# Optimization experiments

Hardware: AMD Instinct MI355X
Metric: run time of the kernel (lower is better)

## Reference

```python
import jax, jax.numpy as jnp
import numpy as np

D_MODEL = 512
KEY_DIM = 128
TEMP = 30.0          # RelationUnit temperature
EPS = 1e-5           # InstanceL2Norm eps
SCALE = float(np.sqrt(1.0 / (D_MODEL * 4 * 4)))  # norm_scale in layers


def _sine_pos(hw, d, dtype=jnp.float32):
    # pos_seq = ones(hw).cumsum() -> 1..hw; outer with inv_freq; cat(sin, cos)
    pos = jnp.arange(1, hw + 1, dtype=dtype)
    inv_freq = 1.0 / (10000.0 ** (jnp.arange(0, d, 2, dtype=dtype) / d))
    ang = pos[:, None] * inv_freq[None, :]          # [hw, d/2]
    return jnp.concatenate([jnp.sin(ang), jnp.cos(ang)], axis=-1)  # [hw, d]


def _attn(q, k, v, wk, bk):
    # Single-head RelationUnit: shared WK projection, L2-normalize, temp softmax, raw value.
    # q: [Lq,B,D], k,v: [Lk,B,D]
    pq = q @ wk.T + bk
    pq = pq / jnp.maximum(jnp.linalg.norm(pq, axis=-1, keepdims=True), 1e-12)
    pk = k @ wk.T + bk
    pk = pk / jnp.maximum(jnp.linalg.norm(pk, axis=-1, keepdims=True), 1e-12)
    logits = jnp.einsum('qbe,kbe->bqk', pq, pk) * TEMP   # [B,Lq,Lk]
    a = jax.nn.softmax(logits, axis=-1)
    return jnp.einsum('bqk,kbd->qbd', a, v)


def _inorm(x, ni, b, d, h, w):
    # InstanceL2Norm (size_average=True) over (d,h,w) per (ni,b) sample.
    y = x.reshape(ni, h, w, b, d)
    ss = jnp.sum(y * y, axis=(1, 2, 4), keepdims=True)
    y = y * (SCALE * jnp.sqrt((d * h * w) / (ss + EPS)))
    return y.reshape(ni * h * w, b, d)


def _flatten(x5):
    # (ni,b,d,h,w) -> (ni*h*w, b, d), matching torch view/permute/reshape order.
    ni, b, d, h, w = x5.shape
    return x5.reshape(ni, b, d, h * w).transpose(0, 3, 1, 2).reshape(ni * h * w, b, d)


def _encoder(src5, pos5, wk, bk):
    ni, b, d, h, w = src5.shape
    x = _flatten(src5) + _flatten(pos5) * 1e-3
    x = x + _attn(x, x, x, wk, bk)
    return _inorm(x, ni, b, d, h, w)


def _decoder_one(tgt5, pos5, memory, pos, wk_s, bk_s, wk_c, bk_c):
    # Single decoder layer on one image (ni == 1).
    ni, b, d, h, w = tgt5.shape
    x = _flatten(tgt5) + _flatten(pos5) * 1e-3
    x = x + _attn(x, x, x, wk_s, bk_s)
    x = _inorm(x, ni, b, d, h, w)
    mask = _attn(x, memory, pos, wk_c, bk_c)
    t2 = _inorm(x * mask, ni, b, d, h, w)
    t3 = _attn(x, memory, memory * pos, wk_c, bk_c)
    t4 = _inorm(x + t3, ni, b, d, h, w)
    x = _inorm(t2 + t4, ni, b, d, h, w)
    return x.reshape(ni, h, w, b, d).transpose(0, 3, 4, 1, 2).reshape(ni * b, d, h, w)


def _forward(train_feat, test_feat, train_label, wk_self, bk_self, wk_cross, bk_cross):
    ntr, b, d, h, w = train_feat.shape
    nte = test_feat.shape[0]
    # Sinusoidal position embedding, reshaped to (d,h,w), broadcast over imgs/batch.
    pe = _sine_pos(h * w, d, train_feat.dtype).reshape(h, w, d).transpose(2, 0, 1)
    train_pos = jnp.broadcast_to(pe, (ntr, b, d, h, w))
    test_pos = jnp.broadcast_to(pe, (nte, b, d, h, w))
    memory = _encoder(train_feat, train_pos, wk_self, bk_self)   # [ntr*h*w, b, d]
    # label -> pos value sequence [ntr*h*w, b, d] (repeated over channel dim)
    pos = train_label.reshape(ntr, b, 1, h * w).transpose(0, 3, 1, 2).reshape(ntr * h * w, b, 1)
    pos = jnp.broadcast_to(pos, (ntr * h * w, b, d))

    def dec(t4, p4):
        return _decoder_one(t4[None], p4[None], memory, pos,
                            wk_self, bk_self, wk_cross, bk_cross)

    enc_feat = jax.vmap(dec)(train_feat, train_pos).reshape(ntr * b, d, h, w)
    dec_feat = jax.vmap(dec)(test_feat, test_pos).reshape(nte * b, d, h, w)
    return enc_feat, dec_feat


def setup_inputs() -> dict:
    key = jax.random.key(0)
    k1, k2, k3, k4, k5 = jax.random.split(key, 5)
    NTR, NTE, B, D, H, W = 3, 3, 16, 512, 22, 22
    std = float(np.sqrt(2.0 / D))  # kaiming-like init for WK
    return {
        'train_feat': jax.random.normal(k1, (NTR, B, D, H, W), jnp.float32),
        'test_feat': jax.random.normal(k2, (NTE, B, D, H, W), jnp.float32),
        'train_label': jax.random.uniform(k3, (NTR, B, H, W), jnp.float32),
        'wk_self': jax.random.normal(k4, (KEY_DIM, D), jnp.float32) * std,
        'bk_self': jnp.zeros((KEY_DIM,), jnp.float32),
        'wk_cross': jax.random.normal(k5, (KEY_DIM, D), jnp.float32) * std,
        'bk_cross': jnp.zeros((KEY_DIM,), jnp.float32),
    }


def reference(train_feat, test_feat, train_label, wk_self, bk_self, wk_cross, bk_cross):
    return _forward(train_feat, test_feat, train_label,
                    wk_self, bk_self, wk_cross, bk_cross)
```

## Files before the change

kernel.cpp:

```cpp
#include <hip/hip_runtime.h>
#include <math.h>

#define BATCH   16
#define DMODEL  512
#define EKEY    128
#define HWSZ    484
#define LENC    1452
#define LKPAD   1536
#define IMG_ELEMS (HWSZ*BATCH*DMODEL)
#define ENC_OUT   11894784ull
#define SQRT_TEMP 5.4772255750516611f
#define INORM_SCALE 0.011048543456039806f
#define NEGBIG   -3.0e38f

typedef _Float16 f16;
typedef _Float16 f16x8 __attribute__((ext_vector_type(8)));
typedef _Float16 f16x4 __attribute__((ext_vector_type(4)));
typedef float    f32x4 __attribute__((ext_vector_type(4)));

__device__ __forceinline__ f32x4 mfma16(f16x8 a, f16x8 b, f32x4 c) {
  return __builtin_amdgcn_mfma_f32_16x16x32_f16(a, b, c, 0, 0, 0);
}
__device__ __forceinline__ float inorm_coef(float ss) {
  return INORM_SCALE * sqrtf(247808.0f / (ss + 1e-5f));
}

#define BARRIER() do { asm volatile("s_waitcnt lgkmcnt(0)" ::: "memory"); \
                       __builtin_amdgcn_s_barrier();                      \
                       asm volatile("" ::: "memory"); } while (0)

__device__ __forceinline__ size_t vfrag_addr(size_t z, int nkt, int d, int k) {
  return (((z * 32 + (d >> 4)) * (size_t)nkt + (k >> 5)) << 9)
         + (((k >> 3) & 3) << 7) + ((d & 15) << 3) + (k & 7);
}

__global__ void init_zero_kernel(float* __restrict__ ss) { ss[threadIdx.x] = 0.0f; }

__global__ void peT_kernel(float* __restrict__ peT) {
  const int c = blockIdx.x;
  const int cc = (c < 256) ? c : c - 256;
  const float invf = 1.0f / powf(10000.0f, (float)(2 * cc) * (1.0f / 512.0f));
  for (int p = threadIdx.x; p < HWSZ; p += blockDim.x) {
    const float ang = (float)(p + 1) * invf;
    peT[c * HWSZ + p] = (c < 256) ? sinf(ang) : cosf(ang);
  }
}

__global__ void build_labelT_kernel(const float* __restrict__ lab, float* __restrict__ labT) {
  const int g = blockIdx.x;
  if (g < 48) {
    const int im = g >> 4, b = g & 15;
    for (int p = threadIdx.x; p < HWSZ; p += blockDim.x)
      labT[(size_t)b * LKPAD + im * HWSZ + p] = lab[((size_t)im * BATCH + b) * HWSZ + p];
  } else {
    const int b = g - 48;
    for (int p = LENC + threadIdx.x; p < LKPAD; p += blockDim.x)
      labT[(size_t)b * LKPAD + p] = 0.0f;
  }
}

__global__ void cvt16_kernel(const float* __restrict__ s, f16* __restrict__ d) {
  const int i = (blockIdx.x * 256 + threadIdx.x) * 4;
  const int r = i >> 9, c = i & 511;
  const float4 v = *(const float4*)(s + i);
  f16x4 h; h[0] = (f16)v.x; h[1] = (f16)v.y; h[2] = (f16)v.z; h[3] = (f16)v.w;
  f16* dp = d + ((((size_t)(r >> 4) << 4) + (c >> 5)) << 9)
              + (((c >> 3) & 3) << 7) + ((r & 15) << 3) + (c & 7);
  *(f16x4*)dp = h;
}

__global__ void vpad_kernel(f16* __restrict__ vt) {
  const int d = blockIdx.x, b = blockIdx.y;
  const int k = LENC + threadIdx.x;
  if (k < LKPAD) vt[vfrag_addr(b, 48, d, k)] = (f16)0.f;
}

__global__ __launch_bounds__(256) void build_input_kernel(
    const float* __restrict__ trainf, const float* __restrict__ testf,
    const float* __restrict__ peT, int i0, float* __restrict__ xout,
    f16* __restrict__ vt, int zmul, int col_im_step, int nkt)
{
  __shared__ float tile[32][33];
  const int tx = threadIdx.x, ty = threadIdx.y;
  const int pt = blockIdx.x * 32, ct = blockIdx.y * 32;
  const int im = blockIdx.z >> 4, b = blockIdx.z & 15;
  const int g = i0 + im;
  const float* src = (g < 3 ? trainf + (size_t)g * IMG_ELEMS
                            : testf + (size_t)(g - 3) * IMG_ELEMS)
                     + (size_t)b * (512 * 484);
  const int zv = zmul ? (im * 16 + b) : b;
  const int col0 = im * col_im_step;
#pragma unroll
  for (int j = 0; j < 4; ++j) {
    const int c = ct + ty + 8 * j, p = pt + tx;
    const int k = col0 + p;
    float val = 0.0f;
    if (p < HWSZ) {
      val = src[(size_t)c * 484 + p] + 1e-3f * peT[(size_t)c * 484 + p];
      vt[vfrag_addr(zv, nkt, c, k)] = (f16)val;
    } else if (zmul) {
      vt[vfrag_addr(zv, nkt, c, k)] = (f16)0.f;
    }
    tile[ty + 8 * j][tx] = val;
  }
  __syncthreads();
#pragma unroll
  for (int j = 0; j < 4; ++j) {
    const int p = pt + ty + 8 * j, c = ct + tx;
    if (p < HWSZ)
      xout[(((size_t)im * HWSZ + p) * BATCH + b) * DMODEL + c] = tile[tx][ty + 8 * j];
  }
}

__global__ __launch_bounds__(256) void v16t_mem_kernel(
    const float* __restrict__ src, const float* __restrict__ ssE, f16* __restrict__ dst)
{
  __shared__ f16 tile[32][33];
  const int tx = threadIdx.x, ty = threadIdx.y;
  const int l0 = blockIdx.x * 32, d0 = blockIdx.y * 32;
  const int b = blockIdx.z;
#pragma unroll
  for (int j = 0; j < 4; ++j) {
    const int l = l0 + ty + 8 * j;
    float v = 0.0f;
    if (l < LENC) {
      const float cf = inorm_coef(ssE[(l / 484) * 16 + b]);
      v = cf * src[((size_t)l * BATCH + b) * DMODEL + d0 + tx];
    }
    tile[ty + 8 * j][tx] = (f16)v;
  }
  __syncthreads();
#pragma unroll
  for (int j = 0; j < 4; ++j) {
    const int d = d0 + ty + 8 * j, l = l0 + tx;
    if (l < LKPAD) dst[vfrag_addr(b, 48, d, l)] = tile[tx][ty + 8 * j];
  }
}

__global__ __launch_bounds__(256) void proj_mfma_kernel(
    const float* __restrict__ X, const f16* __restrict__ W16,
    const float* __restrict__ bias, const float* __restrict__ ssg,
    f16* __restrict__ P16, int L, int NLT)
{
  __shared__ f16 Xs[64][72];
  const int t = threadIdx.x;
  const int wave = t >> 6, lane = t & 63, quad = lane >> 4, ln = lane & 15;
  const int lane8 = lane * 8;
  const size_t row0 = (size_t)blockIdx.x * 64;

  f32x4 acc[8];
#pragma unroll
  for (int nt = 0; nt < 8; ++nt) acc[nt] = (f32x4){0.f, 0.f, 0.f, 0.f};

  const int sr = t >> 2, sko = (t & 3) * 16;
  const size_t rowg = row0 + sr;
  float cf = 1.0f;
  if (ssg) {
    const int bb = (int)(rowg & 15);
    const int gg = (int)((rowg >> 4) / 484);
    cf = inorm_coef(ssg[gg * 16 + bb]);
  }
  const float* xp = X + rowg * 512 + sko;

  for (int k0 = 0; k0 < 512; k0 += 64) {
    {
      const float4 a0 = *(const float4*)(xp + k0);
      const float4 a1 = *(const float4*)(xp + k0 + 4);
      const float4 a2 = *(const float4*)(xp + k0 + 8);
      const float4 a3 = *(const float4*)(xp + k0 + 12);
      f16x8 h0, h1;
      h0[0]=(f16)(cf*a0.x); h0[1]=(f16)(cf*a0.y); h0[2]=(f16)(cf*a0.z); h0[3]=(f16)(cf*a0.w);
      h0[4]=(f16)(cf*a1.x); h0[5]=(f16)(cf*a1.y); h0[6]=(f16)(cf*a1.z); h0[7]=(f16)(cf*a1.w);
      h1[0]=(f16)(cf*a2.x); h1[1]=(f16)(cf*a2.y); h1[2]=(f16)(cf*a2.z); h1[3]=(f16)(cf*a2.w);
      h1[4]=(f16)(cf*a3.x); h1[5]=(f16)(cf*a3.y); h1[6]=(f16)(cf*a3.z); h1[7]=(f16)(cf*a3.w);
      *(f16x8*)&Xs[sr][sko]     = h0;
      *(f16x8*)&Xs[sr][sko + 8] = h1;
    }
    __syncthreads();
#pragma unroll
    for (int ks = 0; ks < 2; ++ks) {
      const f16x8 a = *(const f16x8*)&Xs[wave * 16 + ln][ks * 32 + quad * 8];
      const int kt = (k0 >> 5) + ks;
#pragma unroll
      for (int nt = 0; nt < 8; ++nt) {
        const f16x8 bf = *(const f16x8*)(W16 + (((size_t)(nt * 16 + kt)) << 9) + lane8);
        acc[nt] = mfma16(a, bf, acc[nt]);
      }
    }
    __syncthreads();
  }

  float bj[8];
#pragma unroll
  for (int nt = 0; nt < 8; ++nt) bj[nt] = bias[nt * 16 + ln];

  float y[8][4]; float ssq[4] = {0.f, 0.f, 0.f, 0.f};
#pragma unroll
  for (int nt = 0; nt < 8; ++nt)
#pragma unroll
    for (int r = 0; r < 4; ++r) {
      const float v = acc[nt][r] + bj[nt];
      y[nt][r] = v; ssq[r] = fmaf(v, v, ssq[r]);
    }
#pragma unroll
  for (int r = 0; r < 4; ++r) {
    ssq[r] += __shfl_xor(ssq[r], 1); ssq[r] += __shfl_xor(ssq[r], 2);
    ssq[r] += __shfl_xor(ssq[r], 4); ssq[r] += __shfl_xor(ssq[r], 8);
  }
#pragma unroll
  for (int r = 0; r < 4; ++r) {
    const float inv = SQRT_TEMP / fmaxf(sqrtf(ssq[r]), 1e-12f);
    const size_t rg = row0 + (size_t)wave * 16 + quad * 4 + r;
    const int b = (int)(rg & 15);
    const size_t lg = rg >> 4;
    const int im = (int)(lg / (size_t)L);
    const int l  = (int)(lg - (size_t)im * L);
    f16* zb = P16 + (((size_t)(im * 16 + b) * NLT + (l >> 4)) << 11) + ((l & 15) << 3) + (ln & 7);
#pragma unroll
    for (int nt = 0; nt < 8; ++nt)
      zb[((size_t)(nt >> 1) << 9) + (((nt * 2 + (ln >> 3)) & 3) << 7)] = (f16)(y[nt][r] * inv);
  }
}

template<int CROSS>
__global__ __launch_bounds__(512) void attn8_kernel(
    const f16* __restrict__ pq, const f16* __restrict__ pk, const f16* __restrict__ Vt,
    const float* __restrict__ labT, float* __restrict__ X, float* __restrict__ Vout,
    const float* __restrict__ ssIn, float* __restrict__ ssO,
    float* __restrict__ ssV_, float* __restrict__ ssUV_,
    int Lq, int Lk, int nqb, int nltq, int nltk, int nktv, int pk_shared, int vt_shared)
{
  __shared__ float Ssm[64][132];
  __shared__ f16   Psm[64][136];
  __shared__ float msh[64], lsh[64], ash[64], mask_sh[64];

  const int t = threadIdx.x;
  const int wave = t >> 6, lane = t & 63, quad = lane >> 4, ln = lane & 15;
  const int lane8 = lane * 8;

  const int id = blockIdx.x;
  const int b  = (id & 7) + 8 * ((id >> 3) & 1);
  const int jj = id >> 4;
  const int qb = jj % nqb, im = jj / nqb;
  const int q0 = qb * 64;
  const int zq = im * 16 + b;
  const int zk = pk_shared ? b : zq;
  const int zv = vt_shared ? b : zq;

  const f16* pqz = pq + (((size_t)zq * nltq) << 11);
  const f16* pkz = pk + (((size_t)zk * nltk) << 11);
  const f16* Vw  = Vt + ((((size_t)zv * 32 + wave * 4) * (size_t)nktv) << 9) + lane8;
  const float* ksb = CROSS ? labT + (size_t)b * LKPAD : (const float*)0;

  f16x8 qf[4][4];
#pragma unroll
  for (int mt = 0; mt < 4; ++mt) {
    const f16* qp = pqz + (((size_t)((q0 >> 4) + mt)) << 11) + lane8;
#pragma unroll
    for (int es = 0; es < 4; ++es) qf[mt][es] = *(const f16x8*)(qp + es * 512);
  }
  f16x8 kf[4];
  {
    const f16* kp = pkz + (((size_t)wave) << 11) + lane8;
#pragma unroll
    for (int es = 0; es < 4; ++es) kf[es] = *(const f16x8*)(kp + es * 512);
  }

  f32x4 oacc[4][4];
#pragma unroll
  for (int mt = 0; mt < 4; ++mt)
#pragma unroll
    for (int nt = 0; nt < 4; ++nt) oacc[mt][nt] = (f32x4){0.f, 0.f, 0.f, 0.f};

  if (t < 64) { msh[t] = NEGBIG; lsh[t] = 0.f; ash[t] = 0.f; }
  float msum = 0.f;
  const int qs = t >> 3, cs = t & 7;
  __syncthreads();

  const int nch = (Lk + 127) >> 7;

  for (int ch = 0; ch < nch; ++ch) {
    const int k0 = ch << 7;
    const int ktb = k0 >> 5;
    f16x8 bvA[4], bvB[4];
#pragma unroll
    for (int nt = 0; nt < 4; ++nt) {
      const f16* vpn = Vw + (((size_t)(nt * nktv + ktb)) << 9);
      bvA[nt] = *(const f16x8*)(vpn);
      bvB[nt] = *(const f16x8*)(vpn + 512);
    }
    float4 lv[4];
    if (CROSS) {
      const float* lp = ksb + k0 + cs * 16;
#pragma unroll
      for (int i = 0; i < 4; ++i) lv[i] = *(const float4*)(lp + i * 4);
    }
    {
      f32x4 s[4];
#pragma unroll
      for (int mt = 0; mt < 4; ++mt) s[mt] = (f32x4){0.f,0.f,0.f,0.f};
      __builtin_amdgcn_s_setprio(1);
#pragma unroll
      for (int es = 0; es < 4; ++es)
#pragma unroll
        for (int mt = 0; mt < 4; ++mt)
          s[mt] = mfma16(qf[mt][es], kf[es], s[mt]);
      __builtin_amdgcn_s_setprio(0);
#pragma unroll
      for (int mt = 0; mt < 4; ++mt)
#pragma unroll
        for (int r = 0; r < 4; ++r)
          Ssm[mt * 16 + quad * 4 + r][wave * 16 + ln] = s[mt][r];
    }
    if (ch + 1 < nch) {
      const f16* kp = pkz + (((size_t)(((ch + 1) << 3) + wave)) << 11) + lane8;
#pragma unroll
      for (int es = 0; es < 4; ++es) kf[es] = *(const f16x8*)(kp + es * 512);
    }
    BARRIER();
    {
      f32x4 sa[4];
#pragma unroll
      for (int i = 0; i < 4; ++i) sa[i] = *(const f32x4*)&Ssm[qs][cs * 16 + i * 4];
      float sv[16];
#pragma unroll
      for (int i = 0; i < 4; ++i)
#pragma unroll
        for (int j = 0; j < 4; ++j)
          sv[i * 4 + j] = sa[i][j];
      if (k0 + 128 > Lk) {
        const int kb = k0 + cs * 16;
#pragma unroll
        for (int j = 0; j < 16; ++j)
          if (kb + j >= Lk) sv[j] = NEGBIG;
      }
      float m8[8];
#pragma unroll
      for (int j = 0; j < 8; ++j) m8[j] = fmaxf(sv[j], sv[j + 8]);
      float m4[4];
#pragma unroll
      for (int j = 0; j < 4; ++j) m4[j] = fmaxf(m8[j], m8[j + 4]);
      float mx = fmaxf(fmaxf(m4[0], m4[2]), fmaxf(m4[1], m4[3]));
      mx = fmaxf(mx, __shfl_xor(mx, 1));
      mx = fmaxf(mx, __shfl_xor(mx, 2));
      mx = fmaxf(mx, __shfl_xor(mx, 4));
      const float mold = msh[qs];
      const float mnew = fmaxf(mold, mx);
      const float alpha = __expf(mold - mnew);
      float ps = 0.f, pm = 0.f;
      f16x8 pv0, pv1;
#pragma unroll
      for (int j = 0; j < 16; ++j) {
        float p = __expf(sv[j] - mnew);
        ps += p;
        if (CROSS) p *= lv[j >> 2][j & 3];
        pm += p;
        if (j < 8) pv0[j] = (f16)p; else pv1[j - 8] = (f16)p;
      }
      *(f16x8*)&Psm[qs][cs * 16]     = pv0;
      *(f16x8*)&Psm[qs][cs * 16 + 8] = pv1;
      ps += __shfl_xor(ps, 1); ps += __shfl_xor(ps, 2); ps += __shfl_xor(ps, 4);
      msum = msum * alpha + pm;
      if (cs == 0) { msh[qs] = mnew; lsh[qs] = lsh[qs] * alpha + ps; ash[qs] = alpha; }
    }
    BARRIER();
    {
      f16x8 bvC[4];
#pragma unroll
      for (int nt = 0; nt < 4; ++nt)
        bvC[nt] = *(const f16x8*)(Vw + (((size_t)(nt * nktv + ktb + 2)) << 9));
#pragma unroll
      for (int mt = 0; mt < 4; ++mt) {
        f32x4 al;
#pragma unroll
        for (int r = 0; r < 4; ++r) al[r] = ash[mt * 16 + quad * 4 + r];
#pragma unroll
        for (int nt = 0; nt < 4; ++nt) oacc[mt][nt] *= al;
      }
      f16x8 pa[4];
#pragma unroll
      for (int mt = 0; mt < 4; ++mt) pa[mt] = *(const f16x8*)&Psm[mt * 16 + ln][quad * 8];
      __builtin_amdgcn_s_setprio(1);
#pragma unroll
      for (int nt = 0; nt < 4; ++nt)
#pragma unroll
        for (int mt = 0; mt < 4; ++mt)
          oacc[mt][nt] = mfma16(pa[mt], bvA[nt], oacc[mt][nt]);
      __builtin_amdgcn_s_setprio(0);
      f16x8 bvD[4];
#pragma unroll
      for (int nt = 0; nt < 4; ++nt)
        bvD[nt] = *(const f16x8*)(Vw + (((size_t)(nt * nktv + ktb + 3)) << 9));
#pragma unroll
      for (int mt = 0; mt < 4; ++mt) pa[mt] = *(const f16x8*)&Psm[mt * 16 + ln][32 + quad * 8];
      __builtin_amdgcn_s_setprio(1);
#pragma unroll
      for (int nt = 0; nt < 4; ++nt)
#pragma unroll
        for (int mt = 0; mt < 4; ++mt)
          oacc[mt][nt] = mfma16(pa[mt], bvB[nt], oacc[mt][nt]);
      __builtin_amdgcn_s_setprio(0);
#pragma unroll
      for (int mt = 0; mt < 4; ++mt) pa[mt] = *(const f16x8*)&Psm[mt * 16 + ln][64 + quad * 8];
      __builtin_amdgcn_s_setprio(1);
#pragma unroll
      for (int nt = 0; nt < 4; ++nt)
#pragma unroll
        for (int mt = 0; mt < 4; ++mt)
          oacc[mt][nt] = mfma16(pa[mt], bvC[nt], oacc[mt][nt]);
      __builtin_amdgcn_s_setprio(0);
#pragma unroll
      for (int mt = 0; mt < 4; ++mt) pa[mt] = *(const f16x8*)&Psm[mt * 16 + ln][96 + quad * 8];
      __builtin_amdgcn_s_setprio(1);
#pragma unroll
      for (int nt = 0; nt < 4; ++nt)
#pragma unroll
        for (int mt = 0; mt < 4; ++mt)
          oacc[mt][nt] = mfma16(pa[mt], bvD[nt], oacc[mt][nt]);
      __builtin_amdgcn_s_setprio(0);
    }
  }

  if (CROSS) {
    float ms = msum;
    ms += __shfl_xor(ms, 1); ms += __shfl_xor(ms, 2); ms += __shfl_xor(ms, 4);
    if (cs == 0) mask_sh[qs] = ms / lsh[qs];
    __syncthreads();
  }

  const int g0  = (im * Lq + q0) / 484;
  const int bhi = (g0 + 1) * 484 - im * Lq;
  const bool strad = (!CROSS) && (bhi < Lq) && (bhi < q0 + 64);

  float a0 = 0.f, a1 = 0.f, a2 = 0.f;
  const float cfA = CROSS ? inorm_coef(ssIn[im * 16 + b]) : 0.f;

#pragma unroll
  for (int mt = 0; mt < 4; ++mt) {
    f32x4 li;
#pragma unroll
    for (int r = 0; r < 4; ++r) li[r] = 1.0f / lsh[mt * 16 + quad * 4 + r];
#pragma unroll
    for (int r = 0; r < 4; ++r) {
      const int q = q0 + mt * 16 + quad * 4 + r;
      if (q < Lq) {
        const size_t base = (((size_t)(im * Lq + q)) * BATCH + b) * DMODEL + wave * 64 + ln;
        if (!CROSS) {
          const bool hi = (q >= bhi);
#pragma unroll
          for (int nt = 0; nt < 4; ++nt) {
            const float y = X[base + nt * 16] + oacc[mt][nt][r] * li[r];
            X[base + nt * 16] = y;
            if (hi) a1 += y * y; else a0 += y * y;
          }
        } else {
          const float mval = mask_sh[mt * 16 + quad * 4 + r];
#pragma unroll
          for (int nt = 0; nt < 4; ++nt) {
            const float x1 = cfA * X[base + nt * 16];
            const float u = x1 * mval;
            const float v = x1 + oacc[mt][nt][r] * li[r];
            X[base + nt * 16] = u;
            Vout[base + nt * 16] = v;
            a0 += u * u; a1 += v * v; a2 += u * v;
          }
        }
      }
    }
  }
#pragma unroll
  for (int m = 32; m; m >>= 1) {
    a0 += __shfl_xor(a0, m); a1 += __shfl_xor(a1, m);
    if (CROSS) a2 += __shfl_xor(a2, m);
  }
  if (lane == 0) {
    if (!CROSS) {
      atomicAdd(ssO + g0 * 16 + b, a0);
      if (strad) atomicAdd(ssO + (g0 + 1) * 16 + b, a1);
    } else {
      const int g = im * 16 + b;
      atomicAdd(ssO + g, a0);
      atomicAdd(ssV_ + g, a1);
      atomicAdd(ssUV_ + g, a2);
    }
  }
}

__global__ void coef_final_kernel(const float* __restrict__ ssU, const float* __restrict__ ssV,
                                  const float* __restrict__ ssUV, float* __restrict__ AB, int n)
{
  const int t = threadIdx.x;
  if (t < n) {
    const float su = ssU[t], sv = ssV[t], suv = ssUV[t];
    const float cu = inorm_coef(su), cv = inorm_coef(sv);
    const float ssz = cu * cu * su + cv * cv * sv + 2.f * cu * cv * suv;
    const float cz = inorm_coef(ssz);
    AB[2 * t] = cu * cz; AB[2 * t + 1] = cv * cz;
  }
}

__global__ __launch_bounds__(256) void final_out_kernel(
    const float* __restrict__ u, const float* __restrict__ v,
    const float* __restrict__ AB, float* __restrict__ out, int i0)
{
  __shared__ float tile[32][33];
  const int tx = threadIdx.x, ty = threadIdx.y;
  const int pt = blockIdx.x * 32, ct = blockIdx.y * 32;
  const int z = blockIdx.z;
  const int im = z >> 4, b = z & 15;
  const float A = AB[2 * z], B = AB[2 * z + 1];
#pragma unroll
  for (int j = 0; j < 4; ++j) {
    const int p = pt + ty + 8 * j, c = ct + tx;
    float val = 0.0f;
    if (p < HWSZ) {
      const size_t idx = (((size_t)im * HWSZ + p) * BATCH + b) * DMODEL + c;
      val = A * u[idx] + B * v[idx];
    }
    tile[ty + 8 * j][tx] = val;
  }
  __syncthreads();
  const int g = i0 + im;
  const size_t base = (g < 3 ? 0ull : ENC_OUT)
                    + ((size_t)(((g < 3 ? g : g - 3) * 16 + b) * 512)) * 484ull;
#pragma unroll
  for (int j = 0; j < 4; ++j) {
    const int c = ct + ty + 8 * j, p = pt + tx;
    if (p < HWSZ) out[base + (size_t)c * 484 + p] = tile[tx][ty + 8 * j];
  }
}

extern "C" void kernel_launch(void* const* d_in, const int* in_sizes, int n_in,
                              void* d_out, int out_size, void* d_ws, size_t ws_size,
                              hipStream_t stream) {
  (void)in_sizes; (void)n_in; (void)out_size;
  const float* train_feat  = (const float*)d_in[0];
  const float* test_feat   = (const float*)d_in[1];
  const float* train_label = (const float*)d_in[2];
  const float* wk_self     = (const float*)d_in[3];
  const float* bk_self     = (const float*)d_in[4];
  const float* wk_cross    = (const float*)d_in[5];
  const float* bk_cross    = (const float*)d_in[6];
  float* out = (float*)d_out;
  char* wsb  = (char*)d_ws;

  size_t off = 0;
  auto alloc = [&](size_t bytes) { size_t r = off; off = (r + bytes + 255) & ~(size_t)255; return r; };
  const size_t o_peT   = alloc(991232ull);
  const size_t o_labT  = alloc(16ull * LKPAD * 4);
  const size_t o_ss    = alloc(4096);
  const size_t o_w16s  = alloc(131072);
  const size_t o_w16c  = alloc(131072);
  const size_t o_xenc  = alloc(47579136ull);
  const size_t o_p16   = alloc(6291456ull);
  const size_t o_vte   = alloc(16ull*512*LKPAD*2);
  const size_t o_vtm   = alloc(16ull*512*LKPAD*2);
  const size_t fixed = off;

  float* peT  = (float*)(wsb + o_peT);
  float* labT = (float*)(wsb + o_labT);
  float* ss   = (float*)(wsb + o_ss);
  f16*   w16s = (f16*)(wsb + o_w16s);
  f16*   w16c = (f16*)(wsb + o_w16c);
  float* xenc = (float*)(wsb + o_xenc);
  f16*   p16  = (f16*)(wsb + o_p16);
  f16*   vte  = (f16*)(wsb + o_vte);
  f16*   vtm  = (f16*)(wsb + o_vtm);
  float* ssE = ss, *ssA = ss + 128, *ssU = ss + 256, *ssV = ss + 384, *ssUV = ss + 512;
  float* AB  = ss + 640;

  const size_t decPer = 15859712ull * 2 + 2097152ull + 8388608ull;
  int NB = 6;
  if (fixed + (size_t)NB * decPer + 4096 > ws_size) NB = 3;
  if (fixed + (size_t)NB * decPer + 4096 > ws_size) NB = 1;

  float* xd    = (float*)(wsb + fixed);
  float* vbuf  = xd + (size_t)NB * IMG_ELEMS;
  f16*   pq16d = (f16*)(vbuf + (size_t)NB * IMG_ELEMS);
  f16*   vtd   = pq16d + (size_t)NB * 1048576ull;

  init_zero_kernel<<<dim3(1), dim3(1024), 0, stream>>>(ss);
  peT_kernel<<<dim3(512), dim3(256), 0, stream>>>(peT);
  build_labelT_kernel<<<dim3(64), dim3(256), 0, stream>>>(train_label, labT);
  cvt16_kernel<<<dim3(64), dim3(256), 0, stream>>>(wk_self, w16s);
  cvt16_kernel<<<dim3(64), dim3(256), 0, stream>>>(wk_cross, w16c);
  vpad_kernel<<<dim3(512, 16), dim3(96), 0, stream>>>(vte);

  build_input_kernel<<<dim3(16, 16, 48), dim3(32, 8), 0, stream>>>(
      train_feat, test_feat, peT, 0, xenc, vte, 0, 484, 48);
  proj_mfma_kernel<<<dim3(363), dim3(256), 0, stream>>>(xenc, w16s, bk_self, (const float*)0, p16, LENC, 96);
  attn8_kernel<0><<<dim3(23 * 16), dim3(512), 0, stream>>>(
      p16, p16, vte, (const float*)0, xenc, (float*)0, (const float*)0,
      ssE, (float*)0, (float*)0, LENC, LENC, 23, 96, 96, 48, 0, 0);
  proj_mfma_kernel<<<dim3(363), dim3(256), 0, stream>>>(xenc, w16c, bk_cross, ssE, p16, LENC, 96);
  v16t_mem_kernel<<<dim3(48, 16, 16), dim3(32, 8), 0, stream>>>(xenc, ssE, vtm);

  for (int i0 = 0; i0 < 6; i0 += NB) {
    build_input_kernel<<<dim3(16, 16, NB * 16), dim3(32, 8), 0, stream>>>(
        train_feat, test_feat, peT, i0, xd, vtd, 1, 0, 16);
    proj_mfma_kernel<<<dim3(NB * 121), dim3(256), 0, stream>>>(xd, w16s, bk_self, (const float*)0, pq16d, HWSZ, 32);
    attn8_kernel<0><<<dim3(8 * 16 * NB), dim3(512), 0, stream>>>(
        pq16d, pq16d, vtd, (const float*)0, xd, (float*)0, (const float*)0,
        ssA + i0 * 16, (float*)0, (float*)0, HWSZ, HWSZ, 8, 32, 32, 16, 0, 0);
    proj_mfma_kernel<<<dim3(NB * 121), dim3(256), 0, stream>>>(xd, w16c, bk_cross, ssA + i0 * 16, pq16d, HWSZ, 32);
    attn8_kernel<1><<<dim3(8 * 16 * NB), dim3(512), 0, stream>>>(
        pq16d, p16 , vtm, labT, xd, vbuf, ssA + i0 * 16,
        ssU + i0 * 16, ssV + i0 * 16, ssUV + i0 * 16, HWSZ, LENC, 8, 32, 96, 48, 1, 1);
    coef_final_kernel<<<dim3(1), dim3(128), 0, stream>>>(
        ssU + i0 * 16, ssV + i0 * 16, ssUV + i0 * 16, AB + i0 * 32, NB * 16);
    final_out_kernel<<<dim3(16, 16, NB * 16), dim3(32, 8), 0, stream>>>(
        xd, vbuf, AB + i0 * 32, out, i0);
  }
}
```

Before: 899.3 us.

## Software-pipeline attention loop with double-buffered score and probability tiles

```diff
diff --git a/kernel.cpp b/kernel.cpp
--- a/kernel.cpp
+++ b/kernel.cpp
@@ -223,16 +223,16 @@
 }
 
 template<int CROSS>
-__global__ __launch_bounds__(512) void attn8_kernel(
+__global__ __launch_bounds__(512) void attn9_kernel(
     const f16* __restrict__ pq, const f16* __restrict__ pk, const f16* __restrict__ Vt,
     const float* __restrict__ labT, float* __restrict__ X, float* __restrict__ Vout,
     const float* __restrict__ ssIn, float* __restrict__ ssO,
     float* __restrict__ ssV_, float* __restrict__ ssUV_,
     int Lq, int Lk, int nqb, int nltq, int nltk, int nktv, int pk_shared, int vt_shared)
 {
-  __shared__ float Ssm[64][132];
-  __shared__ f16   Psm[64][136];
-  __shared__ float msh[64], lsh[64], ash[64], mask_sh[64];
+  __shared__ float Ssm[2][64][132];
+  __shared__ f16   Psm[2][64][136];
+  __shared__ float msh[64], lsh[64], ash[2][64], mask_sh[64];
 
   const int t = threadIdx.x;
   const int wave = t >> 6, lane = t & 63, quad = lane >> 4, ln = lane & 15;
@@ -272,30 +272,119 @@
 #pragma unroll
     for (int nt = 0; nt < 4; ++nt) oacc[mt][nt] = (f32x4){0.f, 0.f, 0.f, 0.f};
 
-  if (t < 64) { msh[t] = NEGBIG; lsh[t] = 0.f; ash[t] = 0.f; }
+  if (t < 64) { msh[t] = NEGBIG; lsh[t] = 0.f; }
   float msum = 0.f;
   const int qs = t >> 3, cs = t & 7;
-  __syncthreads();
 
   const int nch = (Lk + 127) >> 7;
 
-  for (int ch = 0; ch < nch; ++ch) {
-    const int k0 = ch << 7;
-    const int ktb = k0 >> 5;
-    f16x8 bvA[4], bvB[4];
-#pragma unroll
-    for (int nt = 0; nt < 4; ++nt) {
-      const f16* vpn = Vw + (((size_t)(nt * nktv + ktb)) << 9);
-      bvA[nt] = *(const f16x8*)(vpn);
-      bvB[nt] = *(const f16x8*)(vpn + 512);
-    }
+  {
+    f32x4 s[4];
+#pragma unroll
+    for (int mt = 0; mt < 4; ++mt) s[mt] = (f32x4){0.f,0.f,0.f,0.f};
+    __builtin_amdgcn_s_setprio(1);
+#pragma unroll
+    for (int es = 0; es < 4; ++es)
+#pragma unroll
+      for (int mt = 0; mt < 4; ++mt)
+        s[mt] = mfma16(qf[mt][es], kf[es], s[mt]);
+    __builtin_amdgcn_s_setprio(0);
+#pragma unroll
+    for (int mt = 0; mt < 4; ++mt)
+#pragma unroll
+      for (int r = 0; r < 4; ++r)
+        Ssm[0][mt * 16 + quad * 4 + r][wave * 16 + ln] = s[mt][r];
+  }
+  if (nch > 1) {
+    const f16* kp = pkz + (((size_t)(8 + wave)) << 11) + lane8;
+#pragma unroll
+    for (int es = 0; es < 4; ++es) kf[es] = *(const f16x8*)(kp + es * 512);
+  }
+  f16x8 bvA[4], bvB[4], bvC[4], bvD[4];
+  BARRIER();
+
+  for (int i = 0; i < nch; ++i) {
+    const int buf = i & 1;
+    const int k0 = i << 7;
+    const int ktb = i << 2;
+    f32x4 sa[4];
+#pragma unroll
+    for (int ii = 0; ii < 4; ++ii) sa[ii] = *(const f32x4*)&Ssm[buf][qs][cs * 16 + ii * 4];
     float4 lv[4];
     if (CROSS) {
       const float* lp = ksb + k0 + cs * 16;
 #pragma unroll
-      for (int i = 0; i < 4; ++i) lv[i] = *(const float4*)(lp + i * 4);
-    }
-    {
+      for (int ii = 0; ii < 4; ++ii) lv[ii] = *(const float4*)(lp + ii * 4);
+    }
+    if (i) {
+#pragma unroll
+      for (int mt = 0; mt < 4; ++mt) {
+        f32x4 al;
+#pragma unroll
+        for (int r = 0; r < 4; ++r) al[r] = ash[buf ^ 1][mt * 16 + quad * 4 + r];
+#pragma unroll
+        for (int nt = 0; nt < 4; ++nt) oacc[mt][nt] *= al;
+      }
+      f16x8 pa[4];
+#pragma unroll
+      for (int mt = 0; mt < 4; ++mt) pa[mt] = *(const f16x8*)&Psm[buf ^ 1][mt * 16 + ln][quad * 8];
+      __builtin_amdgcn_s_setprio(1);
+#pragma unroll
+      for (int nt = 0; nt < 4; ++nt)
+#pragma unroll
+        for (int mt = 0; mt < 4; ++mt)
+          oacc[mt][nt] = mfma16(pa[mt], bvA[nt], oacc[mt][nt]);
+      __builtin_amdgcn_s_setprio(0);
+#pragma unroll
+      for (int nt = 0; nt < 4; ++nt)
+        bvA[nt] = *(const f16x8*)(Vw + (((size_t)(nt * nktv + ktb)) << 9));
+#pragma unroll
+      for (int mt = 0; mt < 4; ++mt) pa[mt] = *(const f16x8*)&Psm[buf ^ 1][mt * 16 + ln][32 + quad * 8];
+      __builtin_amdgcn_s_setprio(1);
+#pragma unroll
+      for (int nt = 0; nt < 4; ++nt)
+#pragma unroll
+        for (int mt = 0; mt < 4; ++mt)
+          oacc[mt][nt] = mfma16(pa[mt], bvB[nt], oacc[mt][nt]);
+      __builtin_amdgcn_s_setprio(0);
+#pragma unroll
+      for (int nt = 0; nt < 4; ++nt)
+        bvB[nt] = *(const f16x8*)(Vw + (((size_t)(nt * nktv + ktb + 1)) << 9));
+#pragma unroll
+      for (int mt = 0; mt < 4; ++mt) pa[mt] = *(const f16x8*)&Psm[buf ^ 1][mt * 16 + ln][64 + quad * 8];
+      __builtin_amdgcn_s_setprio(1);
+#pragma unroll
+      for (int nt = 0; nt < 4; ++nt)
+#pragma unroll
+        for (int mt = 0; mt < 4; ++mt)
+          oacc[mt][nt] = mfma16(pa[mt], bvC[nt], oacc[mt][nt]);
+      __builtin_amdgcn_s_setprio(0);
+#pragma unroll
+      for (int nt = 0; nt < 4; ++nt)
+        bvC[nt] = *(const f16x8*)(Vw + (((size_t)(nt * nktv + ktb + 2)) << 9));
+#pragma unroll
+      for (int mt = 0; mt < 4; ++mt) pa[mt] = *(const f16x8*)&Psm[buf ^ 1][mt * 16 + ln][96 + quad * 8];
+      __builtin_amdgcn_s_setprio(1);
+#pragma unroll
+      for (int nt = 0; nt < 4; ++nt)
+#pragma unroll
+        for (int mt = 0; mt < 4; ++mt)
+          oacc[mt][nt] = mfma16(pa[mt], bvD[nt], oacc[mt][nt]);
+      __builtin_amdgcn_s_setprio(0);
+#pragma unroll
+      for (int nt = 0; nt < 4; ++nt)
+        bvD[nt] = *(const f16x8*)(Vw + (((size_t)(nt * nktv + ktb + 3)) << 9));
+    } else {
+#pragma unroll
+      for (int nt = 0; nt < 4; ++nt) {
+        const f16* vpn = Vw + (((size_t)(nt * nktv)) << 9);
+        bvA[nt] = *(const f16x8*)(vpn);
+        bvB[nt] = *(const f16x8*)(vpn + 512);
+        bvC[nt] = *(const f16x8*)(vpn + 1024);
+        bvD[nt] = *(const f16x8*)(vpn + 1536);
+      }
+    }
+    if (i + 1 < nch) {
       f32x4 s[4];
 #pragma unroll
       for (int mt = 0; mt < 4; ++mt) s[mt] = (f32x4){0.f,0.f,0.f,0.f};
@@ -310,24 +399,20 @@
       for (int mt = 0; mt < 4; ++mt)
 #pragma unroll
         for (int r = 0; r < 4; ++r)
-          Ssm[mt * 16 + quad * 4 + r][wave * 16 + ln] = s[mt][r];
-    }
-    if (ch + 1 < nch) {
-      const f16* kp = pkz + (((size_t)(((ch + 1) << 3) + wave)) << 11) + lane8;
-#pragma unroll
-      for (int es = 0; es < 4; ++es) kf[es] = *(const f16x8*)(kp + es * 512);
-    }
-    BARRIER();
+          Ssm[buf ^ 1][mt * 16 + quad * 4 + r][wave * 16 + ln] = s[mt][r];
+      if (i + 2 < nch) {
+        const f16* kp = pkz + (((size_t)(((i + 2) << 3) + wave)) << 11) + lane8;
+#pragma unroll
+        for (int es = 0; es < 4; ++es) kf[es] = *(const f16x8*)(kp + es * 512);
+      }
+    }
     {
-      f32x4 sa[4];
-#pragma unroll
-      for (int i = 0; i < 4; ++i) sa[i] = *(const f32x4*)&Ssm[qs][cs * 16 + i * 4];
       float sv[16];
 #pragma unroll
-      for (int i = 0; i < 4; ++i)
+      for (int ii = 0; ii < 4; ++ii)
 #pragma unroll
         for (int j = 0; j < 4; ++j)
-          sv[i * 4 + j] = sa[i][j];
+          sv[ii * 4 + j] = sa[ii][j];
       if (k0 + 128 > Lk) {
         const int kb = k0 + cs * 16;
 #pragma unroll
@@ -357,66 +442,38 @@
         pm += p;
         if (j < 8) pv0[j] = (f16)p; else pv1[j - 8] = (f16)p;
       }
-      *(f16x8*)&Psm[qs][cs * 16]     = pv0;
-      *(f16x8*)&Psm[qs][cs * 16 + 8] = pv1;
+      *(f16x8*)&Psm[buf][qs][cs * 16]     = pv0;
+      *(f16x8*)&Psm[buf][qs][cs * 16 + 8] = pv1;
       ps += __shfl_xor(ps, 1); ps += __shfl_xor(ps, 2); ps += __shfl_xor(ps, 4);
       msum = msum * alpha + pm;
-      if (cs == 0) { msh[qs] = mnew; lsh[qs] = lsh[qs] * alpha + ps; ash[qs] = alpha; }
+      if (cs == 0) { msh[qs] = mnew; lsh[qs] = lsh[qs] * alpha + ps; ash[buf][qs] = alpha; }
     }
     BARRIER();
-    {
-      f16x8 bvC[4];
-#pragma unroll
-      for (int nt = 0; nt < 4; ++nt)
-        bvC[nt] = *(const f16x8*)(Vw + (((size_t)(nt * nktv + ktb + 2)) << 9));
-#pragma unroll
-      for (int mt = 0; mt < 4; ++mt) {
-        f32x4 al;
-#pragma unroll
-        for (int r = 0; r < 4; ++r) al[r] = ash[mt * 16 + quad * 4 + r];
-#pragma unroll
-        for (int nt = 0; nt < 4; ++nt) oacc[mt][nt] *= al;
-      }
-      f16x8 pa[4];
-#pragma unroll
-      for (int mt = 0; mt < 4; ++mt) pa[mt] = *(const f16x8*)&Psm[mt * 16 + ln][quad * 8];
+  }
+
+  {
+    const int bl = (nch - 1) & 1;
+#pragma unroll
+    for (int mt = 0; mt < 4; ++mt) {
+      f32x4 al;
+#pragma unroll
+      for (int r = 0; r < 4; ++r) al[r] = ash[bl][mt * 16 + quad * 4 + r];
+#pragma unroll
+      for (int nt = 0; nt < 4; ++nt) oacc[mt][nt] *= al;
+    }
+    f16x8 pa[4];
+#pragma unroll
+    for (int ks = 0; ks < 4; ++ks) {
+#pragma unroll
+      for (int mt = 0; mt < 4; ++mt) pa[mt] = *(const f16x8*)&Psm[bl][mt * 16 + ln][ks * 32 + quad * 8];
       __builtin_amdgcn_s_setprio(1);
 #pragma unroll
-      for (int nt = 0; nt < 4; ++nt)
+      for (int nt = 0; nt < 4; ++nt) {
+        const f16x8 bv = (ks == 0) ? bvA[nt] : (ks == 1) ? bvB[nt] : (ks == 2) ? bvC[nt] : bvD[nt];
 #pragma unroll
         for (int mt = 0; mt < 4; ++mt)
-          oacc[mt][nt] = mfma16(pa[mt], bvA[nt], oacc[mt][nt]);
-      __builtin_amdgcn_s_setprio(0);
-      f16x8 bvD[4];
-#pragma unroll
-      for (int nt = 0; nt < 4; ++nt)
-        bvD[nt] = *(const f16x8*)(Vw + (((size_t)(nt * nktv + ktb + 3)) << 9));
-#pragma unroll
-      for (int mt = 0; mt < 4; ++mt) pa[mt] = *(const f16x8*)&Psm[mt * 16 + ln][32 + quad * 8];
-      __builtin_amdgcn_s_setprio(1);
-#pragma unroll
-      for (int nt = 0; nt < 4; ++nt)
-#pragma unroll
-        for (int mt = 0; mt < 4; ++mt)
-          oacc[mt][nt] = mfma16(pa[mt], bvB[nt], oacc[mt][nt]);
-      __builtin_amdgcn_s_setprio(0);
-#pragma unroll
-      for (int mt = 0; mt < 4; ++mt) pa[mt] = *(const f16x8*)&Psm[mt * 16 + ln][64 + quad * 8];
-      __builtin_amdgcn_s_setprio(1);
-#pragma unroll
-      for (int nt = 0; nt < 4; ++nt)
-#pragma unroll
-        for (int mt = 0; mt < 4; ++mt)
-          oacc[mt][nt] = mfma16(pa[mt], bvC[nt], oacc[mt][nt]);
-      __builtin_amdgcn_s_setprio(0);
-#pragma unroll
-      for (int mt = 0; mt < 4; ++mt) pa[mt] = *(const f16x8*)&Psm[mt * 16 + ln][96 + quad * 8];
-      __builtin_amdgcn_s_setprio(1);
-#pragma unroll
-      for (int nt = 0; nt < 4; ++nt)
-#pragma unroll
-        for (int mt = 0; mt < 4; ++mt)
-          oacc[mt][nt] = mfma16(pa[mt], bvD[nt], oacc[mt][nt]);
+          oacc[mt][nt] = mfma16(pa[mt], bv, oacc[mt][nt]);
+      }
       __builtin_amdgcn_s_setprio(0);
     }
   }
@@ -589,7 +646,7 @@
   build_input_kernel<<<dim3(16, 16, 48), dim3(32, 8), 0, stream>>>(
       train_feat, test_feat, peT, 0, xenc, vte, 0, 484, 48);
   proj_mfma_kernel<<<dim3(363), dim3(256), 0, stream>>>(xenc, w16s, bk_self, (const float*)0, p16, LENC, 96);
-  attn8_kernel<0><<<dim3(23 * 16), dim3(512), 0, stream>>>(
+  attn9_kernel<0><<<dim3(23 * 16), dim3(512), 0, stream>>>(
       p16, p16, vte, (const float*)0, xenc, (float*)0, (const float*)0,
       ssE, (float*)0, (float*)0, LENC, LENC, 23, 96, 96, 48, 0, 0);
   proj_mfma_kernel<<<dim3(363), dim3(256), 0, stream>>>(xenc, w16c, bk_cross, ssE, p16, LENC, 96);
@@ -599,11 +656,11 @@
     build_input_kernel<<<dim3(16, 16, NB * 16), dim3(32, 8), 0, stream>>>(
         train_feat, test_feat, peT, i0, xd, vtd, 1, 0, 16);
     proj_mfma_kernel<<<dim3(NB * 121), dim3(256), 0, stream>>>(xd, w16s, bk_self, (const float*)0, pq16d, HWSZ, 32);
-    attn8_kernel<0><<<dim3(8 * 16 * NB), dim3(512), 0, stream>>>(
+    attn9_kernel<0><<<dim3(8 * 16 * NB), dim3(512), 0, stream>>>(
         pq16d, pq16d, vtd, (const float*)0, xd, (float*)0, (const float*)0,
         ssA + i0 * 16, (float*)0, (float*)0, HWSZ, HWSZ, 8, 32, 32, 16, 0, 0);
     proj_mfma_kernel<<<dim3(NB * 121), dim3(256), 0, stream>>>(xd, w16c, bk_cross, ssA + i0 * 16, pq16d, HWSZ, 32);
-    attn8_kernel<1><<<dim3(8 * 16 * NB), dim3(512), 0, stream>>>(
+    attn9_kernel<1><<<dim3(8 * 16 * NB), dim3(512), 0, stream>>>(
         pq16d, p16 , vtm, labT, xd, vbuf, ssA + i0 * 16,
         ssU + i0 * 16, ssV + i0 * 16, ssUV + i0 * 16, HWSZ, LENC, 8, 32, 96, 48, 1, 1);
     coef_final_kernel<<<dim3(1), dim3(128), 0, stream>>>(
```

Measured after the change: 1.027 ms. 14.2% more time.
